# Performance work log

Hardware: AMD Instinct MI355X
Metric: run time of the kernel (lower is better)

Reference implementation:

```python
import jax, jax.numpy as jnp
import numpy as np

N_NODES = 50000
N_GRAPHS = 128
N_FEATS = 128
HIDDEN = 128
FC_HID = 64
N_CLASSES = 10
N_EDGES = 600000


def gcn_conv(x, W, b, src, dst, n):
    # x: [N, Fin] -> [N, Fout]; symmetric-normalized scatter aggregation (PyG GCNConv)
    h = x @ W  # [N, Fout]
    ones = jnp.ones(src.shape[0], dtype=h.dtype)
    deg = jax.ops.segment_sum(ones, dst, num_segments=n)  # in-degree incl. self loops
    dinv = jnp.where(deg > 0, jax.lax.rsqrt(jnp.maximum(deg, 1.0)), 0.0)
    norm = dinv[src] * dinv[dst]  # [E]
    msg = norm[:, None] * h[src]  # gather + scale, [E, Fout]
    out = jax.ops.segment_sum(msg, dst, num_segments=n)  # scatter-add
    return out + b


def setup_inputs() -> dict:
    key = jax.random.key(0)
    ks = jax.random.split(key, 16)
    x = jax.random.normal(ks[0], (N_NODES, N_FEATS), dtype=jnp.float32)
    edge_index = jax.random.randint(ks[1], (2, N_EDGES), 0, N_NODES, dtype=jnp.int64)
    batch = jnp.sort(jax.random.randint(ks[2], (N_NODES,), 0, N_GRAPHS, dtype=jnp.int64))

    def lin(k, fin, fout):
        s = 1.0 / np.sqrt(fin)
        kw, kb = jax.random.split(k)
        W = jax.random.uniform(kw, (fin, fout), jnp.float32, -s, s)
        b = jax.random.uniform(kb, (fout,), jnp.float32, -s, s)
        return W, b

    W1, b1 = lin(ks[3], N_FEATS, HIDDEN)
    W2, b2 = lin(ks[4], HIDDEN, HIDDEN)
    W3, b3 = lin(ks[5], HIDDEN, HIDDEN)
    Wf1, bf1 = lin(ks[6], HIDDEN, FC_HID)
    Wf2, bf2 = lin(ks[7], FC_HID, N_CLASSES)
    return {"x": x, "edge_index": edge_index, "batch": batch,
            "W1": W1, "b1": b1, "W2": W2, "b2": b2, "W3": W3, "b3": b3,
            "Wf1": Wf1, "bf1": bf1, "Wf2": Wf2, "bf2": bf2}


def reference(x, edge_index, batch, W1, b1, W2, b2, W3, b3, Wf1, bf1, Wf2, bf2):
    n = x.shape[0]
    # add self loops (PyG GCNConv default)
    loop = jnp.arange(n, dtype=edge_index.dtype)
    src = jnp.concatenate([edge_index[0], loop])
    dst = jnp.concatenate([edge_index[1], loop])

    h = jax.nn.relu(gcn_conv(x, W1, b1, src, dst, n))
    h = jax.nn.relu(gcn_conv(h, W2, b2, src, dst, n))
    h = jax.nn.relu(gcn_conv(h, W3, b3, src, dst, n))

    # global mean pool per graph
    sums = jax.ops.segment_sum(h, batch, num_segments=N_GRAPHS)
    cnts = jax.ops.segment_sum(jnp.ones((n,), h.dtype), batch, num_segments=N_GRAPHS)
    hg = sums / jnp.maximum(cnts, 1.0)[:, None]  # [G, HIDDEN]

    h = jax.nn.relu(hg @ Wf1 + bf1)
    return h @ Wf2 + bf2  # [G, N_CLASSES]
```

## Files before the change

### kernel.cpp

```cpp
#include <hip/hip_runtime.h>

#define NFEAT 128
#define NGRAPHS 128
#define FCH 64
#define NCLS 10
#define ELLW 48

__global__ void ell_fill_kernel(const int* __restrict__ src, const int* __restrict__ dst, int E,
                                int* __restrict__ cursor, int* __restrict__ ell) {
    int i = (blockIdx.x * blockDim.x + threadIdx.x) * 4;
    if (i + 3 < E) {
        int4 s4 = *(const int4*)(src + i);
        int4 d4 = *(const int4*)(dst + i);
        int p;
        p = atomicAdd(&cursor[d4.x], 1); if (p < ELLW) ell[(size_t)d4.x * ELLW + p] = s4.x;
        p = atomicAdd(&cursor[d4.y], 1); if (p < ELLW) ell[(size_t)d4.y * ELLW + p] = s4.y;
        p = atomicAdd(&cursor[d4.z], 1); if (p < ELLW) ell[(size_t)d4.z * ELLW + p] = s4.z;
        p = atomicAdd(&cursor[d4.w], 1); if (p < ELLW) ell[(size_t)d4.w * ELLW + p] = s4.w;
    } else {
        for (int j = i; j < E; ++j) {
            int d = dst[j];
            int p = atomicAdd(&cursor[d], 1);
            if (p < ELLW) ell[(size_t)d * ELLW + p] = src[j];
        }
    }
}

__global__ void dinv_kernel(const int* __restrict__ deg, float* __restrict__ dinv, int N) {
    int i = blockIdx.x * blockDim.x + threadIdx.x;
    if (i < N) dinv[i] = rsqrtf((float)(deg[i] + 1));
}

__global__ __launch_bounds__(256)
void gemm128_kernel(const float* __restrict__ X, const float* __restrict__ W,
                    const float* __restrict__ dinv, float* __restrict__ H, int N) {
    __shared__ float4 Ws4[64 * 32];
    int t = threadIdx.x;
    int tx = t & 15;
    int ty = t >> 4;
    int r0 = blockIdx.x * 64 + ty * 4;

    const float* xr[4];
    bool rowok[4];
    #pragma unroll
    for (int i = 0; i < 4; ++i) {
        rowok[i] = (r0 + i < N);
        xr[i] = X + (size_t)(rowok[i] ? (r0 + i) : 0) * NFEAT;
    }

    float acc[4][8];
    #pragma unroll
    for (int i = 0; i < 4; ++i)
        #pragma unroll
        for (int j = 0; j < 8; ++j) acc[i][j] = 0.f;

    const float4* W4 = (const float4*)W;

    #pragma unroll
    for (int ph = 0; ph < 2; ++ph) {
        #pragma unroll
        for (int i = 0; i < 8; ++i) Ws4[t + i * 256] = W4[ph * 2048 + t + i * 256];
        __syncthreads();

        for (int k = 0; k < 64; k += 4) {
            float xk[4][4];
            #pragma unroll
            for (int i = 0; i < 4; ++i) {
                float4 v = *(const float4*)(xr[i] + ph * 64 + k);
                xk[i][0] = v.x; xk[i][1] = v.y; xk[i][2] = v.z; xk[i][3] = v.w;
            }
            #pragma unroll
            for (int kk = 0; kk < 4; ++kk) {
                float4 wa = Ws4[(k + kk) * 32 + tx];
                float4 wb = Ws4[(k + kk) * 32 + 16 + tx];
                float w[8] = {wa.x, wa.y, wa.z, wa.w, wb.x, wb.y, wb.z, wb.w};
                #pragma unroll
                for (int i = 0; i < 4; ++i) {
                    float xv = xk[i][kk];
                    #pragma unroll
                    for (int j = 0; j < 8; ++j) acc[i][j] = fmaf(xv, w[j], acc[i][j]);
                }
            }
        }
        __syncthreads();
    }

    #pragma unroll
    for (int i = 0; i < 4; ++i) {
        if (rowok[i]) {
            float di = dinv[r0 + i];
            float* hp = H + (size_t)(r0 + i) * NFEAT;
            float4 o0 = {di * acc[i][0], di * acc[i][1], di * acc[i][2], di * acc[i][3]};
            float4 o1 = {di * acc[i][4], di * acc[i][5], di * acc[i][6], di * acc[i][7]};
            *(float4*)(hp + tx * 4) = o0;
            *(float4*)(hp + 64 + tx * 4) = o1;
        }
    }
}

__global__ __launch_bounds__(256)
void aggregate_kernel(const float* __restrict__ Hs, const int* __restrict__ deg,
                      const int* __restrict__ ell, const float* __restrict__ dinv,
                      const float* __restrict__ bias, float* __restrict__ out, int N) {
    int node = (blockIdx.x * 256 + threadIdx.x) >> 6;
    int lane = threadIdx.x & 63;
    if (node >= N) return;

    int half = lane >> 5;
    int fl = lane & 31;
    const float4* H4 = (const float4*)Hs;

    float di = dinv[node];
    float4 acc = {0.f, 0.f, 0.f, 0.f};
    if (half == 0) acc = H4[(size_t)node * 32 + fl];

    const int* row = ell + (size_t)node * ELLW;
    int d = deg[node]; if (d > ELLW) d = ELLW;
    int e = 0;

    for (; e + 7 < d; e += 8) {
        int s0 = row[e + half], s1 = row[e + 2 + half];
        int s2 = row[e + 4 + half], s3 = row[e + 6 + half];
        float4 v0 = H4[(size_t)s0 * 32 + fl];
        float4 v1 = H4[(size_t)s1 * 32 + fl];
        float4 v2 = H4[(size_t)s2 * 32 + fl];
        float4 v3 = H4[(size_t)s3 * 32 + fl];
        acc.x += v0.x + v1.x + v2.x + v3.x;
        acc.y += v0.y + v1.y + v2.y + v3.y;
        acc.z += v0.z + v1.z + v2.z + v3.z;
        acc.w += v0.w + v1.w + v2.w + v3.w;
    }
    for (; e + 1 < d; e += 2) {
        int s = row[e + half];
        float4 v = H4[(size_t)s * 32 + fl];
        acc.x += v.x; acc.y += v.y; acc.z += v.z; acc.w += v.w;
    }
    if (e < d && half == 0) {
        int s = row[e];
        float4 v = H4[(size_t)s * 32 + fl];
        acc.x += v.x; acc.y += v.y; acc.z += v.z; acc.w += v.w;
    }

    acc.x += __shfl_down(acc.x, 32, 64);
    acc.y += __shfl_down(acc.y, 32, 64);
    acc.z += __shfl_down(acc.z, 32, 64);
    acc.w += __shfl_down(acc.w, 32, 64);

    if (half == 0) {
        float4 b = ((const float4*)bias)[fl];
        float4 o;
        o.x = fmaxf(fmaf(di, acc.x, b.x), 0.f);
        o.y = fmaxf(fmaf(di, acc.y, b.y), 0.f);
        o.z = fmaxf(fmaf(di, acc.z, b.z), 0.f);
        o.w = fmaxf(fmaf(di, acc.w, b.w), 0.f);
        ((float4*)(out + (size_t)node * NFEAT))[fl] = o;
    }
}

__global__ __launch_bounds__(256)
void poolfc_kernel(const float* __restrict__ H, const int* __restrict__ batch, int N,
                   const float* __restrict__ Wf1, const float* __restrict__ bf1,
                   const float* __restrict__ Wf2, const float* __restrict__ bf2,
                   float* __restrict__ out) {
    int g = blockIdx.x;

    int lo = 0, hi = N;
    while (lo < hi) { int mid = (lo + hi) >> 1; if (batch[mid] < g) lo = mid + 1; else hi = mid; }
    int start = lo;
    hi = N;
    while (lo < hi) { int mid = (lo + hi) >> 1; if (batch[mid] < g + 1) lo = mid + 1; else hi = mid; }
    int end = lo;

    int wave = threadIdx.x >> 6;
    int lane = threadIdx.x & 63;

    float2 acc = {0.f, 0.f};
    for (int i = start + wave; i < end; i += 4) {
        float2 v = ((const float2*)(H + (size_t)i * NFEAT))[lane];
        acc.x += v.x; acc.y += v.y;
    }

    __shared__ float2 part[4][64];
    __shared__ float hg[NFEAT];
    __shared__ float h1[FCH];
    part[wave][lane] = acc;
    __syncthreads();

    if (wave == 0) {
        float2 t0 = part[0][lane], t1 = part[1][lane], t2 = part[2][lane], t3 = part[3][lane];
        float c = fmaxf((float)(end - start), 1.0f);
        hg[lane * 2]     = (t0.x + t1.x + t2.x + t3.x) / c;
        hg[lane * 2 + 1] = (t0.y + t1.y + t2.y + t3.y) / c;
        float a = bf1[lane];
        #pragma unroll 4
        for (int k = 0; k < NFEAT; ++k) a = fmaf(hg[k], Wf1[k * FCH + lane], a);
        h1[lane] = fmaxf(a, 0.f);
        if (lane < NCLS) {
            float o = bf2[lane];
            #pragma unroll
            for (int j = 0; j < FCH; ++j) o = fmaf(h1[j], Wf2[j * NCLS + lane], o);
            out[g * NCLS + lane] = o;
        }
    }
}

extern "C" void kernel_launch(void* const* d_in, const int* in_sizes, int n_in,
                              void* d_out, int out_size, void* d_ws, size_t ws_size,
                              hipStream_t stream) {
    const float* x   = (const float*)d_in[0];
    const int*   ei  = (const int*)d_in[1];
    const int*   bat = (const int*)d_in[2];
    const float* W1  = (const float*)d_in[3];
    const float* b1  = (const float*)d_in[4];
    const float* W2  = (const float*)d_in[5];
    const float* b2  = (const float*)d_in[6];
    const float* W3  = (const float*)d_in[7];
    const float* b3  = (const float*)d_in[8];
    const float* Wf1 = (const float*)d_in[9];
    const float* bf1 = (const float*)d_in[10];
    const float* Wf2 = (const float*)d_in[11];
    const float* bf2 = (const float*)d_in[12];
    float* out = (float*)d_out;

    int N = in_sizes[0] / NFEAT;
    int E = in_sizes[1] / 2;
    const int* src = ei;
    const int* dst = ei + E;

    char* ws = (char*)d_ws;
    size_t off = 0;
    auto align256 = [](size_t v) { return (v + 255) & ~(size_t)255; };

    int* cursor = (int*)(ws + off);
    off = align256(off + (size_t)N * 4);
    int* ell = (int*)(ws + off);
    off = align256(off + (size_t)N * ELLW * 4);
    float* dinv = (float*)(ws + off);
    off = align256(off + (size_t)N * 4);
    float* h0 = (float*)(ws + off);
    off = align256(off + (size_t)N * NFEAT * 4);
    float* h1 = (float*)(ws + off);
    off = align256(off + (size_t)N * NFEAT * 4);

    hipMemsetAsync(cursor, 0, (size_t)N * 4, stream);

    int tpb = 256;
    int e4blocks = ((E + 3) / 4 + tpb - 1) / tpb;
    int nblocks = (N + tpb - 1) / tpb;

    ell_fill_kernel<<<e4blocks, tpb, 0, stream>>>(src, dst, E, cursor, ell);
    dinv_kernel<<<nblocks, tpb, 0, stream>>>(cursor, dinv, N);

    int gemm_blocks = (N + 63) / 64;
    int agg_blocks = (N + 3) / 4;

    gemm128_kernel<<<gemm_blocks, 256, 0, stream>>>(x, W1, dinv, h0, N);
    aggregate_kernel<<<agg_blocks, 256, 0, stream>>>(h0, cursor, ell, dinv, b1, h1, N);
    gemm128_kernel<<<gemm_blocks, 256, 0, stream>>>(h1, W2, dinv, h0, N);
    aggregate_kernel<<<agg_blocks, 256, 0, stream>>>(h0, cursor, ell, dinv, b2, h1, N);
    gemm128_kernel<<<gemm_blocks, 256, 0, stream>>>(h1, W3, dinv, h0, N);
    aggregate_kernel<<<agg_blocks, 256, 0, stream>>>(h0, cursor, ell, dinv, b3, h1, N);

    poolfc_kernel<<<NGRAPHS, 256, 0, stream>>>(h1, bat, N, Wf1, bf1, Wf2, bf2, out);
}
```

Measured before the change: 390.4 us.

## Fuse aggregation and GEMM per layer by aggregating first, then multiplying in shared memory

Each GCN layer becomes one kernel. Neighbour features are first aggregated with per-source dinv scaling into a shared-memory tile of 64 rows, and that tile is then multiplied by W, with bias and ReLU applied at the end. This uses the identity A(XW) = (AX)W and removes the intermediate H write and read plus half of the launches. In exchange, every gathered edge now needs an extra dinv load, and each block holds 64 rows and about 50KB of shared memory, which may reduce occupancy and latency hiding for the gather phase. The final layer now writes to h0, so poolfc reads from h0.

```diff
diff --git a/kernel.cpp b/kernel.cpp
--- a/kernel.cpp
+++ b/kernel.cpp
@@ -5,6 +5,8 @@
 #define FCH 64
 #define NCLS 10
 #define ELLW 48
+#define BROWS 64
+#define XPAD 132
 
 __global__ void ell_fill_kernel(const int* __restrict__ src, const int* __restrict__ dst, int E,
                                 int* __restrict__ cursor, int* __restrict__ ell) {
@@ -32,128 +34,144 @@
 }
 
 __global__ __launch_bounds__(256)
-void gemm128_kernel(const float* __restrict__ X, const float* __restrict__ W,
-                    const float* __restrict__ dinv, float* __restrict__ H, int N) {
-    __shared__ float4 Ws4[64 * 32];
+void layer_kernel(const float* __restrict__ In, const float* __restrict__ W,
+                  const float* __restrict__ dinvv, const int* __restrict__ deg,
+                  const int* __restrict__ ell, const float* __restrict__ bias,
+                  float* __restrict__ Out, int N) {
+    __shared__ float Xs[BROWS * XPAD];
+    __shared__ float4 Ws4[32 * 32];
     int t = threadIdx.x;
-    int tx = t & 15;
-    int ty = t >> 4;
-    int r0 = blockIdx.x * 64 + ty * 4;
-
-    const float* xr[4];
-    bool rowok[4];
-    #pragma unroll
-    for (int i = 0; i < 4; ++i) {
-        rowok[i] = (r0 + i < N);
-        xr[i] = X + (size_t)(rowok[i] ? (r0 + i) : 0) * NFEAT;
-    }
-
-    float acc[4][8];
-    #pragma unroll
-    for (int i = 0; i < 4; ++i)
+    int n0 = blockIdx.x * BROWS;
+
+    {
+        int wave = t >> 6;
+        int lane = t & 63;
+        int half = lane >> 5;
+        int fl = lane & 31;
+        const float4* H4 = (const float4*)In;
+
+        #pragma unroll 1
+        for (int i = 0; i < BROWS / 4 / 4; ++i) {
+        }
+        #pragma unroll 1
+        for (int i = 0; i < 16; ++i) {
+            int node = n0 + wave * 16 + i;
+            if (node >= N) break;
+
+            float di = dinvv[node];
+            float4 acc = {0.f, 0.f, 0.f, 0.f};
+            if (half == 0) {
+                float4 h = H4[(size_t)node * 32 + fl];
+                acc.x = di * h.x; acc.y = di * h.y; acc.z = di * h.z; acc.w = di * h.w;
+            }
+
+            const int* row = ell + (size_t)node * ELLW;
+            int d = deg[node]; if (d > ELLW) d = ELLW;
+            int e = 0;
+
+            for (; e + 7 < d; e += 8) {
+                int s0 = row[e + half], s1 = row[e + 2 + half];
+                int s2 = row[e + 4 + half], s3 = row[e + 6 + half];
+                float d0 = dinvv[s0], d1 = dinvv[s1], d2 = dinvv[s2], d3 = dinvv[s3];
+                float4 v0 = H4[(size_t)s0 * 32 + fl];
+                float4 v1 = H4[(size_t)s1 * 32 + fl];
+                float4 v2 = H4[(size_t)s2 * 32 + fl];
+                float4 v3 = H4[(size_t)s3 * 32 + fl];
+                acc.x = fmaf(d0, v0.x, acc.x); acc.y = fmaf(d0, v0.y, acc.y);
+                acc.z = fmaf(d0, v0.z, acc.z); acc.w = fmaf(d0, v0.w, acc.w);
+                acc.x = fmaf(d1, v1.x, acc.x); acc.y = fmaf(d1, v1.y, acc.y);
+                acc.z = fmaf(d1, v1.z, acc.z); acc.w = fmaf(d1, v1.w, acc.w);
+                acc.x = fmaf(d2, v2.x, acc.x); acc.y = fmaf(d2, v2.y, acc.y);
+                acc.z = fmaf(d2, v2.z, acc.z); acc.w = fmaf(d2, v2.w, acc.w);
+                acc.x = fmaf(d3, v3.x, acc.x); acc.y = fmaf(d3, v3.y, acc.y);
+                acc.z = fmaf(d3, v3.z, acc.z); acc.w = fmaf(d3, v3.w, acc.w);
+            }
+            for (; e + 1 < d; e += 2) {
+                int s = row[e + half];
+                float ds = dinvv[s];
+                float4 v = H4[(size_t)s * 32 + fl];
+                acc.x = fmaf(ds, v.x, acc.x); acc.y = fmaf(ds, v.y, acc.y);
+                acc.z = fmaf(ds, v.z, acc.z); acc.w = fmaf(ds, v.w, acc.w);
+            }
+            if (e < d && half == 0) {
+                int s = row[e];
+                float ds = dinvv[s];
+                float4 v = H4[(size_t)s * 32 + fl];
+                acc.x = fmaf(ds, v.x, acc.x); acc.y = fmaf(ds, v.y, acc.y);
+                acc.z = fmaf(ds, v.z, acc.z); acc.w = fmaf(ds, v.w, acc.w);
+            }
+
+            acc.x += __shfl_down(acc.x, 32, 64);
+            acc.y += __shfl_down(acc.y, 32, 64);
+            acc.z += __shfl_down(acc.z, 32, 64);
+            acc.w += __shfl_down(acc.w, 32, 64);
+
+            if (half == 0) {
+                float4 o = {di * acc.x, di * acc.y, di * acc.z, di * acc.w};
+                *(float4*)(&Xs[(wave * 16 + i) * XPAD + fl * 4]) = o;
+            }
+        }
+    }
+    __syncthreads();
+
+    {
+        int tx = t & 15;
+        int ty = t >> 4;
+        int rl0 = ty * 4;
+        int r0 = n0 + rl0;
+
+        float acc[4][8];
         #pragma unroll
-        for (int j = 0; j < 8; ++j) acc[i][j] = 0.f;
-
-    const float4* W4 = (const float4*)W;
-
-    #pragma unroll
-    for (int ph = 0; ph < 2; ++ph) {
-        #pragma unroll
-        for (int i = 0; i < 8; ++i) Ws4[t + i * 256] = W4[ph * 2048 + t + i * 256];
-        __syncthreads();
-
-        for (int k = 0; k < 64; k += 4) {
-            float xk[4][4];
+        for (int i = 0; i < 4; ++i)
             #pragma unroll
-            for (int i = 0; i < 4; ++i) {
-                float4 v = *(const float4*)(xr[i] + ph * 64 + k);
-                xk[i][0] = v.x; xk[i][1] = v.y; xk[i][2] = v.z; xk[i][3] = v.w;
-            }
+            for (int j = 0; j < 8; ++j) acc[i][j] = 0.f;
+
+        const float4* W4g = (const float4*)W;
+
+        #pragma unroll 1
+        for (int c = 0; c < 4; ++c) {
             #pragma unroll
-            for (int kk = 0; kk < 4; ++kk) {
-                float4 wa = Ws4[(k + kk) * 32 + tx];
-                float4 wb = Ws4[(k + kk) * 32 + 16 + tx];
-                float w[8] = {wa.x, wa.y, wa.z, wa.w, wb.x, wb.y, wb.z, wb.w};
+            for (int j = 0; j < 4; ++j) Ws4[t + j * 256] = W4g[c * 1024 + t + j * 256];
+            __syncthreads();
+
+            #pragma unroll 2
+            for (int k = 0; k < 32; k += 4) {
+                float xk[4][4];
                 #pragma unroll
                 for (int i = 0; i < 4; ++i) {
-                    float xv = xk[i][kk];
+                    float4 v = *(const float4*)(&Xs[(rl0 + i) * XPAD + c * 32 + k]);
+                    xk[i][0] = v.x; xk[i][1] = v.y; xk[i][2] = v.z; xk[i][3] = v.w;
+                }
+                #pragma unroll
+                for (int kk = 0; kk < 4; ++kk) {
+                    float4 wa = Ws4[(k + kk) * 32 + tx];
+                    float4 wb = Ws4[(k + kk) * 32 + 16 + tx];
+                    float w[8] = {wa.x, wa.y, wa.z, wa.w, wb.x, wb.y, wb.z, wb.w};
                     #pragma unroll
-                    for (int j = 0; j < 8; ++j) acc[i][j] = fmaf(xv, w[j], acc[i][j]);
+                    for (int i = 0; i < 4; ++i) {
+                        float xv = xk[i][kk];
+                        #pragma unroll
+                        for (int j = 0; j < 8; ++j) acc[i][j] = fmaf(xv, w[j], acc[i][j]);
+                    }
                 }
             }
-        }
-        __syncthreads();
-    }
-
-    #pragma unroll
-    for (int i = 0; i < 4; ++i) {
-        if (rowok[i]) {
-            float di = dinv[r0 + i];
-            float* hp = H + (size_t)(r0 + i) * NFEAT;
-            float4 o0 = {di * acc[i][0], di * acc[i][1], di * acc[i][2], di * acc[i][3]};
-            float4 o1 = {di * acc[i][4], di * acc[i][5], di * acc[i][6], di * acc[i][7]};
-            *(float4*)(hp + tx * 4) = o0;
-            *(float4*)(hp + 64 + tx * 4) = o1;
-        }
-    }
-}
-
-__global__ __launch_bounds__(256)
-void aggregate_kernel(const float* __restrict__ Hs, const int* __restrict__ deg,
-                      const int* __restrict__ ell, const float* __restrict__ dinv,
-                      const float* __restrict__ bias, float* __restrict__ out, int N) {
-    int node = (blockIdx.x * 256 + threadIdx.x) >> 6;
-    int lane = threadIdx.x & 63;
-    if (node >= N) return;
-
-    int half = lane >> 5;
-    int fl = lane & 31;
-    const float4* H4 = (const float4*)Hs;
-
-    float di = dinv[node];
-    float4 acc = {0.f, 0.f, 0.f, 0.f};
-    if (half == 0) acc = H4[(size_t)node * 32 + fl];
-
-    const int* row = ell + (size_t)node * ELLW;
-    int d = deg[node]; if (d > ELLW) d = ELLW;
-    int e = 0;
-
-    for (; e + 7 < d; e += 8) {
-        int s0 = row[e + half], s1 = row[e + 2 + half];
-        int s2 = row[e + 4 + half], s3 = row[e + 6 + half];
-        float4 v0 = H4[(size_t)s0 * 32 + fl];
-        float4 v1 = H4[(size_t)s1 * 32 + fl];
-        float4 v2 = H4[(size_t)s2 * 32 + fl];
-        float4 v3 = H4[(size_t)s3 * 32 + fl];
-        acc.x += v0.x + v1.x + v2.x + v3.x;
-        acc.y += v0.y + v1.y + v2.y + v3.y;
-        acc.z += v0.z + v1.z + v2.z + v3.z;
-        acc.w += v0.w + v1.w + v2.w + v3.w;
-    }
-    for (; e + 1 < d; e += 2) {
-        int s = row[e + half];
-        float4 v = H4[(size_t)s * 32 + fl];
-        acc.x += v.x; acc.y += v.y; acc.z += v.z; acc.w += v.w;
-    }
-    if (e < d && half == 0) {
-        int s = row[e];
-        float4 v = H4[(size_t)s * 32 + fl];
-        acc.x += v.x; acc.y += v.y; acc.z += v.z; acc.w += v.w;
-    }
-
-    acc.x += __shfl_down(acc.x, 32, 64);
-    acc.y += __shfl_down(acc.y, 32, 64);
-    acc.z += __shfl_down(acc.z, 32, 64);
-    acc.w += __shfl_down(acc.w, 32, 64);
-
-    if (half == 0) {
-        float4 b = ((const float4*)bias)[fl];
-        float4 o;
-        o.x = fmaxf(fmaf(di, acc.x, b.x), 0.f);
-        o.y = fmaxf(fmaf(di, acc.y, b.y), 0.f);
-        o.z = fmaxf(fmaf(di, acc.z, b.z), 0.f);
-        o.w = fmaxf(fmaf(di, acc.w, b.w), 0.f);
-        ((float4*)(out + (size_t)node * NFEAT))[fl] = o;
+            __syncthreads();
+        }
+
+        float4 ba = ((const float4*)bias)[tx];
+        float4 bb = ((const float4*)bias)[16 + tx];
+        #pragma unroll
+        for (int i = 0; i < 4; ++i) {
+            if (r0 + i < N) {
+                float* hp = Out + (size_t)(r0 + i) * NFEAT;
+                float4 o0 = {fmaxf(acc[i][0] + ba.x, 0.f), fmaxf(acc[i][1] + ba.y, 0.f),
+                             fmaxf(acc[i][2] + ba.z, 0.f), fmaxf(acc[i][3] + ba.w, 0.f)};
+                float4 o1 = {fmaxf(acc[i][4] + bb.x, 0.f), fmaxf(acc[i][5] + bb.y, 0.f),
+                             fmaxf(acc[i][6] + bb.z, 0.f), fmaxf(acc[i][7] + bb.w, 0.f)};
+                *(float4*)(hp + tx * 4) = o0;
+                *(float4*)(hp + 64 + tx * 4) = o1;
+            }
+        }
     }
 }
 
@@ -251,15 +269,11 @@
     ell_fill_kernel<<<e4blocks, tpb, 0, stream>>>(src, dst, E, cursor, ell);
     dinv_kernel<<<nblocks, tpb, 0, stream>>>(cursor, dinv, N);
 
-    int gemm_blocks = (N + 63) / 64;
-    int agg_blocks = (N + 3) / 4;
-
-    gemm128_kernel<<<gemm_blocks, 256, 0, stream>>>(x, W1, dinv, h0, N);
-    aggregate_kernel<<<agg_blocks, 256, 0, stream>>>(h0, cursor, ell, dinv, b1, h1, N);
-    gemm128_kernel<<<gemm_blocks, 256, 0, stream>>>(h1, W2, dinv, h0, N);
-    aggregate_kernel<<<agg_blocks, 256, 0, stream>>>(h0, cursor, ell, dinv, b2, h1, N);
-    gemm128_kernel<<<gemm_blocks, 256, 0, stream>>>(h1, W3, dinv, h0, N);
-    aggregate_kernel<<<agg_blocks, 256, 0, stream>>>(h0, cursor, ell, dinv, b3, h1, N);
-
-    poolfc_kernel<<<NGRAPHS, 256, 0, stream>>>(h1, bat, N, Wf1, bf1, Wf2, bf2, out);
-}
+    int layer_blocks = (N + BROWS - 1) / BROWS;
+
+    layer_kernel<<<layer_blocks, 256, 0, stream>>>(x,  W1, dinv, cursor, ell, b1, h0, N);
+    layer_kernel<<<layer_blocks, 256, 0, stream>>>(h0, W2, dinv, cursor, ell, b2, h1, N);
+    layer_kernel<<<layer_blocks, 256, 0, stream>>>(h1, W3, dinv, cursor, ell, b3, h0, N);
+
+    poolfc_kernel<<<NGRAPHS, 256, 0, stream>>>(h0, bat, N, Wf1, bf1, Wf2, bf2, out);
+}
```

Measured after the change: 485.4 us. 24.3% more time.
